# Performance work log

Measured on AMD Instinct MI355X. Metric: run time of the kernel, lower is better.

The kernel has to match this reference:

```python
import jax, jax.numpy as jnp
import numpy as np

D_MODEL = 1024
N_HEADS = 16
D_K = 64  # per-head dim and the scaling denominator used by the module
NEG = -1e9  # stand-in for -inf in masked_fill (rows are never fully masked)


def setup_inputs() -> dict:
    key = jax.random.key(0)
    ks = jax.random.split(key, 8)
    B, M, N = 2, 2048, 2048
    q = jax.random.normal(ks[0], (B, M, D_MODEL), dtype=jnp.float32)
    k = jax.random.normal(ks[1], (B, N, D_MODEL), dtype=jnp.float32)
    v = jax.random.normal(ks[2], (B, N, D_MODEL), dtype=jnp.float32)
    mask = jax.random.randint(ks[3], (B, M, N), 0, 2).astype(jnp.bool_)
    # xavier_uniform for square [d,d] weights: limit = sqrt(6/(d+d))
    lim = float(np.sqrt(6.0 / (D_MODEL + D_MODEL)))
    Wq = jax.random.uniform(ks[4], (D_MODEL, D_MODEL), jnp.float32, -lim, lim)
    Wk = jax.random.uniform(ks[5], (D_MODEL, D_MODEL), jnp.float32, -lim, lim)
    Wv = jax.random.uniform(ks[6], (D_MODEL, D_MODEL), jnp.float32, -lim, lim)
    Wo = jax.random.uniform(ks[7], (D_MODEL, D_MODEL), jnp.float32, -lim, lim)
    return {"q": q, "k": k, "v": v, "mask": mask,
            "Wq": Wq, "Wk": Wk, "Wv": Wv, "Wo": Wo}


def _split_heads(x):
    # (B, S, D) -> (B, H, S, Dh); the torch split/cat-on-batch trick is
    # mathematically identical to this standard head reshape.
    B, S, _ = x.shape
    return x.reshape(B, S, N_HEADS, D_K).transpose(0, 2, 1, 3)


def reference(q, k, v, mask, Wq, Wk, Wv, Wo):
    qw = _split_heads(q @ Wq.T)  # (B,H,M,Dh)
    kw = _split_heads(k @ Wk.T)  # (B,H,N,Dh)
    vw = _split_heads(v @ Wv.T)  # (B,H,N,Dh)
    scores = jnp.einsum('bhmd,bhnd->bhmn', qw, kw)
    scores = jnp.where(mask[:, None, :, :], NEG, scores)
    attn = jax.nn.softmax(scores / jnp.sqrt(jnp.float32(D_K)), axis=-1)
    ctx = jnp.einsum('bhmn,bhnd->bhmd', attn, vw)
    B, _, M, _ = ctx.shape
    ctx = ctx.transpose(0, 2, 1, 3).reshape(B, M, D_MODEL)
    return ctx @ Wo.T
```

## Files before the change

### kernel.cpp

```cpp
#include <hip/hip_runtime.h>
#include <hip/hip_bf16.h>
#include <stdint.h>
#include <string.h>

#define SEQ   2048
#define DM    1024
#define NH    16
#define NB    2

typedef __attribute__((ext_vector_type(8))) short bf16x8;
typedef __attribute__((ext_vector_type(4))) float f32x4;
typedef unsigned short u16;
typedef unsigned int   u32;

__device__ __forceinline__ u16 f2bf(float f) {
    u32 u = __float_as_uint(f);
    u += 0x7FFF + ((u >> 16) & 1);
    return (u16)(u >> 16);
}
__device__ __forceinline__ u32 pk2bf(float a, float b) {
    __hip_bfloat162 p = __float22bfloat162_rn(make_float2(a, b));
    u32 u; memcpy(&u, &p, 4); return u;
}
__device__ __forceinline__ float fexp2(float x) {
#if __has_builtin(__builtin_amdgcn_exp2f)
    return __builtin_amdgcn_exp2f(x);
#else
    return exp2f(x);
#endif
}
__device__ __forceinline__ void gl_lds16(const void* g, void* l) {
    __builtin_amdgcn_global_load_lds(
        (const __attribute__((address_space(1))) u32*)g,
        (__attribute__((address_space(3))) u32*)l, 16, 0, 0);
}
__device__ __forceinline__ void wbar_vm3() { asm volatile("s_waitcnt vmcnt(3)\ns_barrier" ::: "memory"); }
__device__ __forceinline__ void wbar_vm4() { asm volatile("s_waitcnt vmcnt(4)\ns_barrier" ::: "memory"); }
__device__ __forceinline__ void wbar_vm6() { asm volatile("s_waitcnt vmcnt(6)\ns_barrier" ::: "memory"); }
__device__ __forceinline__ void vm_drain() { asm volatile("s_waitcnt vmcnt(0)" ::: "memory"); }

struct CvtArgs {
    const float* s[7];
    u16* d[7];
    float scale[7];
    int start[8];
};
__global__ __launch_bounds__(256) void cvt_kernel(CvtArgs a) {
    int bid = blockIdx.x;
    int seg = 0;
#pragma unroll
    for (int i = 1; i < 7; ++i) if (bid >= a.start[i]) seg = i;
    float sc = a.scale[seg];
    size_t base = (size_t)(bid - a.start[seg]) * 2048 + threadIdx.x * 8;
    const float4* s4 = (const float4*)(a.s[seg] + base);
    float4 x = s4[0], y = s4[1];
    u32 r[4];
    r[0] = pk2bf(x.x*sc, x.y*sc); r[1] = pk2bf(x.z*sc, x.w*sc);
    r[2] = pk2bf(y.x*sc, y.y*sc); r[3] = pk2bf(y.z*sc, y.w*sc);
    *(uint4*)(a.d[seg] + base) = *(uint4*)r;
}

__global__ void maskpack_kernel(const int* __restrict__ mask,
                                unsigned int* __restrict__ bits) {
    int gid = blockIdx.x * 256 + threadIdx.x;
    int m = mask[gid];
    unsigned long long bal = __ballot(m != 0);
    int lane = threadIdx.x & 63;
    if (lane == 0)       bits[gid >> 5] = (u32)(bal & 0xFFFFFFFFull);
    else if (lane == 32) bits[gid >> 5] = (u32)(bal >> 32);
}

template<int RT>
__device__ __forceinline__ void gemm_body(const u16* __restrict__ A,
                                          const u16* __restrict__ Bm,
                                          void* __restrict__ Y,
                                          int rtile, int ctile, int mode,
                                          u16* sA, u16* sB) {
    constexpr int ABUF = RT * 32 * 32;
    constexpr int BBUF = 128 * 32;
    const int tid  = threadIdx.x;
    const int wv   = tid >> 6, lane = tid & 63;
    const int quad = lane >> 4, ln = lane & 15;
    const int wr   = wv >> 1,  wc  = wv & 1;

    const int lr4 = lane >> 2;
    const int lcc = ((lane & 3) ^ ((lane >> 3) & 3)) * 8;

    const u16* gA[RT/2]; u16* lA[RT/2];
#pragma unroll
    for (int s = 0; s < RT/2; ++s) {
        int seg = wv * (RT/2) + s;
        gA[s] = A + (size_t)(rtile * (RT*32) + seg*16 + lr4) * 1024 + lcc;
        lA[s] = sA + seg * 512;
    }
    const u16* gB[2]; u16* lB[2];
#pragma unroll
    for (int s = 0; s < 2; ++s) {
        int seg = wv * 2 + s;
        gB[s] = Bm + (size_t)(ctile * 128 + seg*16 + lr4) * 1024 + lcc;
        lB[s] = sB + seg * 512;
    }

    f32x4 acc[RT][4];
#pragma unroll
    for (int i = 0; i < RT; ++i)
#pragma unroll
        for (int j = 0; j < 4; ++j) acc[i][j] = (f32x4){0.f,0.f,0.f,0.f};

    const int c0 = (quad ^ ((ln >> 1) & 3)) * 8;

#pragma unroll
    for (int s = 0; s < RT/2; ++s) gl_lds16(gA[s], lA[s]);
#pragma unroll
    for (int s = 0; s < 2; ++s)    gl_lds16(gB[s], lB[s]);
#pragma unroll
    for (int s = 0; s < RT/2; ++s) gl_lds16(gA[s] + 32, lA[s] + ABUF);
#pragma unroll
    for (int s = 0; s < 2; ++s)    gl_lds16(gB[s] + 32, lB[s] + BBUF);

    int bc = 0, bp = 2;
    for (int kt = 0; kt < 32; ++kt) {
        if (RT == 4) wbar_vm4(); else wbar_vm3();
        int pk = (kt + 2) & 31;
#pragma unroll
        for (int s = 0; s < RT/2; ++s) gl_lds16(gA[s] + pk*32, lA[s] + bp*ABUF);
#pragma unroll
        for (int s = 0; s < 2; ++s)    gl_lds16(gB[s] + pk*32, lB[s] + bp*BBUF);

        const u16* sAb = sA + bc * ABUF;
        const u16* sBb = sB + bc * BBUF;
        bf16x8 af[RT], bfr[4];
#pragma unroll
        for (int rt = 0; rt < RT; ++rt)
            af[rt] = *(const bf16x8*)(sAb + (wr*(RT*16) + rt*16 + ln) * 32 + c0);
#pragma unroll
        for (int ct = 0; ct < 4; ++ct)
            bfr[ct] = *(const bf16x8*)(sBb + (wc*64 + ct*16 + ln) * 32 + c0);
#pragma unroll
        for (int rt = 0; rt < RT; ++rt)
#pragma unroll
            for (int ct = 0; ct < 4; ++ct)
                acc[rt][ct] = __builtin_amdgcn_mfma_f32_16x16x32_bf16(
                    af[rt], bfr[ct], acc[rt][ct], 0, 0, 0);

        bc = (bc == 2) ? 0 : bc + 1;
        bp = (bp == 2) ? 0 : bp + 1;
    }
    vm_drain();

#pragma unroll
    for (int rt = 0; rt < RT; ++rt) {
#pragma unroll
        for (int ct = 0; ct < 4; ++ct) {
#pragma unroll
            for (int i = 0; i < 4; ++i) {
                int R = rtile*(RT*32) + wr*(RT*16) + rt*16 + quad*4 + i;
                int C = ctile*128 + wc*64 + ct*16 + ln;
                float val = acc[rt][ct][i];
                if (mode == 0) {
                    int b = R >> 11, s = R & 2047, h = C >> 6, d = C & 63;
                    ((u16*)Y)[((size_t)((b*NH + h) * SEQ + s) << 6) + d] = f2bf(val);
                } else if (mode == 1) {
                    int h = R >> 6, d = R & 63, b = C >> 11, n = C & 2047;
                    ((u16*)Y)[((size_t)((b*NH + h) * 64 + d) << 11) + n] = f2bf(val);
                } else {
                    ((float*)Y)[(size_t)R * 1024 + C] = val;
                }
            }
        }
    }
}

struct QKVArgs { const u16* A[3]; const u16* B[3]; u16* Y[3]; };

__global__ __launch_bounds__(256) void gemm_qkv(QKVArgs g) {
    __shared__ u16 sA[3 * 128 * 32];
    __shared__ u16 sB[3 * 128 * 32];
    int z = blockIdx.z;
    if (z == 2)
        gemm_body<4>(g.A[2], g.B[2], g.Y[2], blockIdx.y, blockIdx.x, 1, sA, sB);
    else
        gemm_body<4>(g.A[z], g.B[z], g.Y[z], blockIdx.x, blockIdx.y, 0, sA, sB);
}

__global__ __launch_bounds__(256) void gemm_out(const u16* __restrict__ A,
                                                const u16* __restrict__ Bm,
                                                float* __restrict__ Y) {
    __shared__ u16 sA[3 * 64 * 32];
    __shared__ u16 sB[3 * 128 * 32];
    gemm_body<2>(A, Bm, Y, blockIdx.x, blockIdx.y, 2, sA, sB);
}

__global__ __launch_bounds__(256) void attn_kernel(
    const u16* __restrict__ qw,
    const u16* __restrict__ kw,
    const u16* __restrict__ vt,
    const u32* __restrict__ mbits,
    u16* __restrict__ ctx) {

    constexpr int RSD = 36;
    __shared__ u16 sK[3 * 4096];
    __shared__ u16 sV[3 * 4096];
    __shared__ u32 sPd[4 * 32 * RSD];

    const int mtile = blockIdx.x;
    const int bh    = blockIdx.y;
    const int b     = bh >> 4;
    const int tid   = threadIdx.x;
    const int wv    = tid >> 6, lane = tid & 63;
    const int quad  = lane >> 4, ln = lane & 15;
    const int m0    = mtile * 128;

    const size_t hbase = (size_t)bh * SEQ * 64;

    bf16x8 qf[2][2];
#pragma unroll
    for (int mt = 0; mt < 2; ++mt) {
        const u16* qp = qw + hbase + (size_t)(m0 + wv*32 + mt*16 + ln) * 64 + quad*8;
        qf[mt][0] = *(const bf16x8*)(qp);
        qf[mt][1] = *(const bf16x8*)(qp + 32);
    }

    f32x4 o[2][4], lsum[2];
#pragma unroll
    for (int mt = 0; mt < 2; ++mt) {
        lsum[mt] = (f32x4){0.f,0.f,0.f,0.f};
#pragma unroll
        for (int j = 0; j < 4; ++j) o[mt][j] = (f32x4){0.f,0.f,0.f,0.f};
    }

    bf16x8 ones;
#pragma unroll
    for (int i = 0; i < 8; ++i) ones[i] = (short)0x3F80;

    const u32* mrow[2];
#pragma unroll
    for (int mt = 0; mt < 2; ++mt)
        mrow[mt] = mbits + (size_t)(b*SEQ + m0 + wv*32 + mt*16 + ln) * 64;

    const int lr = lane >> 3;
    const int lc = (lane & 7) ^ lr;
    const u16* gK[2]; const u16* gV[2];
    u16 *lK[2], *lV[2];
#pragma unroll
    for (int s = 0; s < 2; ++s) {
        int seg = s * 4 + wv;
        gK[s] = kw + hbase + (size_t)(seg*8 + lr) * 64 + lc*8;
        gV[s] = vt + hbase + (size_t)(seg*8 + lr) * SEQ + lc*8;
        lK[s] = sK + seg * 512;
        lV[s] = sV + seg * 512;
    }

    const int c0 = (quad ^ (ln & 7)) * 8;
    u32* sPw = sPd + wv * 32 * RSD;
    const u16* sP16 = (const u16*)sPd;

#pragma unroll
    for (int s = 0; s < 2; ++s) { gl_lds16(gK[s], lK[s]); gl_lds16(gV[s], lV[s]); }
    uint2 wwA[2], wwB[2], wwC[2];
#pragma unroll
    for (int mt = 0; mt < 2; ++mt) wwA[mt] = *(const uint2*)(mrow[mt]);
#pragma unroll
    for (int s = 0; s < 2; ++s) {
        gl_lds16(gK[s] + 4096, lK[s] + 4096);
        gl_lds16(gV[s] + 64,   lV[s] + 4096);
    }
#pragma unroll
    for (int mt = 0; mt < 2; ++mt) wwB[mt] = *(const uint2*)(mrow[mt] + 2);

    int bc = 0, bp = 2;
    for (int nt = 0; nt < SEQ / 64; ++nt) {
        wbar_vm6();
        int pidx = (nt + 2) & 31;
#pragma unroll
        for (int s = 0; s < 2; ++s) {
            gl_lds16(gK[s] + (size_t)pidx * 4096, lK[s] + bp*4096);
            gl_lds16(gV[s] + pidx * 64,           lV[s] + bp*4096);
        }
#pragma unroll
        for (int mt = 0; mt < 2; ++mt)
            wwC[mt] = *(const uint2*)(mrow[mt] + pidx*2);

        const u16* sKb = sK + bc * 4096;
        const u16* sVb = sV + bc * 4096;

        f32x4 s4[2][4];
#pragma unroll
        for (int ct = 0; ct < 4; ++ct) {
            const u16* kp = sKb + (ct*16 + ln) * 64;
            bf16x8 k0 = *(const bf16x8*)(kp + c0);
            bf16x8 k1 = *(const bf16x8*)(kp + (c0 ^ 32));
#pragma unroll
            for (int mt = 0; mt < 2; ++mt) {
                f32x4 z = (f32x4){0.f, 0.f, 0.f, 0.f};
                z = __builtin_amdgcn_mfma_f32_16x16x32_bf16(k0, qf[mt][0], z, 0, 0, 0);
                z = __builtin_amdgcn_mfma_f32_16x16x32_bf16(k1, qf[mt][1], z, 0, 0, 0);
                s4[mt][ct] = z;
            }
        }

#pragma unroll
        for (int mt = 0; mt < 2; ++mt) {
            u32 w0 = wwA[mt].x >> (quad * 4);
            u32 w1 = wwA[mt].y >> (quad * 4);
#pragma unroll
            for (int ct = 0; ct < 4; ++ct) {
                u32 wsel = (ct & 2) ? w1 : w0;
                float p[4];
#pragma unroll
                for (int i = 0; i < 4; ++i) {
                    bool msk = (wsel >> ((ct & 1) * 16 + i)) & 1u;
                    p[i] = fexp2(msk ? -1e9f : s4[mt][ct][i]);
                }
                uint2 pk;
                pk.x = pk2bf(p[0], p[1]);
                pk.y = pk2bf(p[2], p[3]);
                *(uint2*)(sPw + (mt*16 + ln) * RSD + ct*8 + quad*2) = pk;
            }
        }

#pragma unroll
        for (int mt = 0; mt < 2; ++mt) {
            const u16* pp = sP16 + (wv*32 + mt*16 + ln) * 72;
            bf16x8 pf0 = *(const bf16x8*)(pp + quad*8);
            bf16x8 pf1 = *(const bf16x8*)(pp + 32 + quad*8);
            lsum[mt] = __builtin_amdgcn_mfma_f32_16x16x32_bf16(pf0, ones, lsum[mt], 0, 0, 0);
            lsum[mt] = __builtin_amdgcn_mfma_f32_16x16x32_bf16(pf1, ones, lsum[mt], 0, 0, 0);
#pragma unroll
            for (int ct = 0; ct < 4; ++ct) {
                const u16* vp = sVb + (ct*16 + ln) * 64;
                bf16x8 v0 = *(const bf16x8*)(vp + c0);
                bf16x8 v1 = *(const bf16x8*)(vp + (c0 ^ 32));
                o[mt][ct] = __builtin_amdgcn_mfma_f32_16x16x32_bf16(pf0, v0, o[mt][ct], 0, 0, 0);
                o[mt][ct] = __builtin_amdgcn_mfma_f32_16x16x32_bf16(pf1, v1, o[mt][ct], 0, 0, 0);
            }
        }

        wwA[0] = wwB[0]; wwA[1] = wwB[1];
        wwB[0] = wwC[0]; wwB[1] = wwC[1];
        bc = (bc == 2) ? 0 : bc + 1;
        bp = (bp == 2) ? 0 : bp + 1;
    }
    vm_drain();

#pragma unroll
    for (int mt = 0; mt < 2; ++mt)
#pragma unroll
        for (int i = 0; i < 4; ++i) {
            float inv = 1.f / lsum[mt][i];
            int m = m0 + wv*32 + mt*16 + quad*4 + i;
            size_t base = ((size_t)(b * SEQ + m) << 10) + (bh & 15) * 64;
#pragma unroll
            for (int ct = 0; ct < 4; ++ct)
                ctx[base + ct*16 + ln] = f2bf(o[mt][ct][i] * inv);
        }
}

extern "C" void kernel_launch(void* const* d_in, const int* in_sizes, int n_in,
                              void* d_out, int out_size, void* d_ws, size_t ws_size,
                              hipStream_t stream) {
    const float* q    = (const float*)d_in[0];
    const float* k    = (const float*)d_in[1];
    const float* v    = (const float*)d_in[2];
    const int*   mask = (const int*)d_in[3];
    const float* Wq   = (const float*)d_in[4];
    const float* Wk   = (const float*)d_in[5];
    const float* Wv   = (const float*)d_in[6];
    const float* Wo   = (const float*)d_in[7];
    float* out = (float*)d_out;

    char* ws = (char*)d_ws;
    const size_t SZH = (size_t)NB * SEQ * DM * 2;
    const size_t SZW = (size_t)DM * DM * 2;
    u16* qw   = (u16*)(ws);
    u16* kw   = (u16*)(ws + SZH);
    u16* vt   = (u16*)(ws + 2*SZH);
    u16* ctx  = (u16*)(ws + 3*SZH);
    u16* vb   = ctx;
    u32* mbits= (u32*)(ws + 4*SZH);
    u16* qb   = (u16*)(ws + 4*SZH + (1u<<20));
    u16* kb   = (u16*)(ws + 4*SZH + (1u<<20) + SZH);
    u16* Wqb  = (u16*)(ws + 4*SZH + (1u<<20) + 2*SZH);
    u16* Wkb  = (u16*)((char*)Wqb + SZW);
    u16* Wvb  = (u16*)((char*)Wqb + 2*SZW);
    u16* Wob  = (u16*)((char*)Wqb + 3*SZW);

    const float CSC = 0.18033688011112042f;

    CvtArgs ca;
    ca.s[0]=q;  ca.d[0]=qb;  ca.scale[0]=1.f;
    ca.s[1]=k;  ca.d[1]=kb;  ca.scale[1]=1.f;
    ca.s[2]=v;  ca.d[2]=vb;  ca.scale[2]=1.f;
    ca.s[3]=Wq; ca.d[3]=Wqb; ca.scale[3]=CSC;
    ca.s[4]=Wk; ca.d[4]=Wkb; ca.scale[4]=1.f;
    ca.s[5]=Wv; ca.d[5]=Wvb; ca.scale[5]=1.f;
    ca.s[6]=Wo; ca.d[6]=Wob; ca.scale[6]=1.f;
    int st[8] = {0, 2048, 4096, 6144, 6656, 7168, 7680, 8192};
    for (int i = 0; i < 8; ++i) ca.start[i] = st[i];
    cvt_kernel<<<dim3(8192), dim3(256), 0, stream>>>(ca);

    maskpack_kernel<<<dim3(NB*SEQ*SEQ/256), dim3(256), 0, stream>>>(mask, mbits);

    QKVArgs ga;
    ga.A[0]=qb;  ga.B[0]=Wqb; ga.Y[0]=qw;
    ga.A[1]=kb;  ga.B[1]=Wkb; ga.Y[1]=kw;
    ga.A[2]=Wvb; ga.B[2]=vb;  ga.Y[2]=vt;
    gemm_qkv<<<dim3(32, 8, 3), dim3(256), 0, stream>>>(ga);

    attn_kernel<<<dim3(SEQ/128, NB*NH), dim3(256), 0, stream>>>(qw, kw, vt, mbits, ctx);

    gemm_out<<<dim3(64, 8), dim3(256), 0, stream>>>(ctx, Wob, out);
}
```

Measured before the change: 276.3 us.

## Shrink attention M-tile to 64, double-buffer K/V, fuse convert and maskpack

The attention kernel now handles 64 query rows per block instead of 128, with one 16-row tile per wave. This doubles the grid to 1024 blocks and reduces registers and LDS per block, aimed at better occupancy and CU fill. The K/V prefetch drops from triple to double buffering, so less latency is hidden and each K/V tile is reused by fewer query rows, which doubles K/V traffic. The fp32-to-bf16 conversion and mask bit-packing kernels are merged into one launch to save a kernel launch and its tail.

```diff
diff --git a/kernel.cpp b/kernel.cpp
--- a/kernel.cpp
+++ b/kernel.cpp
@@ -34,9 +34,9 @@
         (const __attribute__((address_space(1))) u32*)g,
         (__attribute__((address_space(3))) u32*)l, 16, 0, 0);
 }
+__device__ __forceinline__ void wbar_vm1() { asm volatile("s_waitcnt vmcnt(1)\ns_barrier" ::: "memory"); }
 __device__ __forceinline__ void wbar_vm3() { asm volatile("s_waitcnt vmcnt(3)\ns_barrier" ::: "memory"); }
 __device__ __forceinline__ void wbar_vm4() { asm volatile("s_waitcnt vmcnt(4)\ns_barrier" ::: "memory"); }
-__device__ __forceinline__ void wbar_vm6() { asm volatile("s_waitcnt vmcnt(6)\ns_barrier" ::: "memory"); }
 __device__ __forceinline__ void vm_drain() { asm volatile("s_waitcnt vmcnt(0)" ::: "memory"); }
 
 struct CvtArgs {
@@ -45,29 +45,30 @@
     float scale[7];
     int start[8];
 };
-__global__ __launch_bounds__(256) void cvt_kernel(CvtArgs a) {
+__global__ __launch_bounds__(256) void prep_kernel(CvtArgs a,
+                                                   const int* __restrict__ mask,
+                                                   u32* __restrict__ bits) {
     int bid = blockIdx.x;
-    int seg = 0;
-#pragma unroll
-    for (int i = 1; i < 7; ++i) if (bid >= a.start[i]) seg = i;
-    float sc = a.scale[seg];
-    size_t base = (size_t)(bid - a.start[seg]) * 2048 + threadIdx.x * 8;
-    const float4* s4 = (const float4*)(a.s[seg] + base);
-    float4 x = s4[0], y = s4[1];
-    u32 r[4];
-    r[0] = pk2bf(x.x*sc, x.y*sc); r[1] = pk2bf(x.z*sc, x.w*sc);
-    r[2] = pk2bf(y.x*sc, y.y*sc); r[3] = pk2bf(y.z*sc, y.w*sc);
-    *(uint4*)(a.d[seg] + base) = *(uint4*)r;
-}
-
-__global__ void maskpack_kernel(const int* __restrict__ mask,
-                                unsigned int* __restrict__ bits) {
-    int gid = blockIdx.x * 256 + threadIdx.x;
-    int m = mask[gid];
-    unsigned long long bal = __ballot(m != 0);
-    int lane = threadIdx.x & 63;
-    if (lane == 0)       bits[gid >> 5] = (u32)(bal & 0xFFFFFFFFull);
-    else if (lane == 32) bits[gid >> 5] = (u32)(bal >> 32);
+    if (bid < 8192) {
+        int seg = 0;
+#pragma unroll
+        for (int i = 1; i < 7; ++i) if (bid >= a.start[i]) seg = i;
+        float sc = a.scale[seg];
+        size_t base = (size_t)(bid - a.start[seg]) * 2048 + threadIdx.x * 8;
+        const float4* s4 = (const float4*)(a.s[seg] + base);
+        float4 x = s4[0], y = s4[1];
+        u32 r[4];
+        r[0] = pk2bf(x.x*sc, x.y*sc); r[1] = pk2bf(x.z*sc, x.w*sc);
+        r[2] = pk2bf(y.x*sc, y.y*sc); r[3] = pk2bf(y.z*sc, y.w*sc);
+        *(uint4*)(a.d[seg] + base) = *(uint4*)r;
+    } else {
+        int gid = (bid - 8192) * 256 + threadIdx.x;
+        int m = mask[gid];
+        unsigned long long bal = __ballot(m != 0);
+        int lane = threadIdx.x & 63;
+        if (lane == 0)       bits[gid >> 5] = (u32)(bal & 0xFFFFFFFFull);
+        else if (lane == 32) bits[gid >> 5] = (u32)(bal >> 32);
+    }
 }
 
 template<int RT>
@@ -198,10 +199,10 @@
     const u32* __restrict__ mbits,
     u16* __restrict__ ctx) {
 
-    constexpr int RSD = 36;
-    __shared__ u16 sK[3 * 4096];
-    __shared__ u16 sV[3 * 4096];
-    __shared__ u32 sPd[4 * 32 * RSD];
+    constexpr int RSD = 34;
+    __shared__ u16 sK[2 * 4096];
+    __shared__ u16 sV[2 * 4096];
+    __shared__ u32 sPd[4 * 16 * RSD];
 
     const int mtile = blockIdx.x;
     const int bh    = blockIdx.y;
@@ -209,34 +210,27 @@
     const int tid   = threadIdx.x;
     const int wv    = tid >> 6, lane = tid & 63;
     const int quad  = lane >> 4, ln = lane & 15;
-    const int m0    = mtile * 128;
+    const int m0    = mtile * 64;
 
     const size_t hbase = (size_t)bh * SEQ * 64;
 
-    bf16x8 qf[2][2];
-#pragma unroll
-    for (int mt = 0; mt < 2; ++mt) {
-        const u16* qp = qw + hbase + (size_t)(m0 + wv*32 + mt*16 + ln) * 64 + quad*8;
-        qf[mt][0] = *(const bf16x8*)(qp);
-        qf[mt][1] = *(const bf16x8*)(qp + 32);
-    }
-
-    f32x4 o[2][4], lsum[2];
-#pragma unroll
-    for (int mt = 0; mt < 2; ++mt) {
-        lsum[mt] = (f32x4){0.f,0.f,0.f,0.f};
-#pragma unroll
-        for (int j = 0; j < 4; ++j) o[mt][j] = (f32x4){0.f,0.f,0.f,0.f};
-    }
+    bf16x8 qf0, qf1;
+    {
+        const u16* qp = qw + hbase + (size_t)(m0 + wv*16 + ln) * 64 + quad*8;
+        qf0 = *(const bf16x8*)(qp);
+        qf1 = *(const bf16x8*)(qp + 32);
+    }
+
+    f32x4 o[4], lsum;
+#pragma unroll
+    for (int j = 0; j < 4; ++j) o[j] = (f32x4){0.f,0.f,0.f,0.f};
+    lsum = (f32x4){0.f,0.f,0.f,0.f};
 
     bf16x8 ones;
 #pragma unroll
     for (int i = 0; i < 8; ++i) ones[i] = (short)0x3F80;
 
-    const u32* mrow[2];
-#pragma unroll
-    for (int mt = 0; mt < 2; ++mt)
-        mrow[mt] = mbits + (size_t)(b*SEQ + m0 + wv*32 + mt*16 + ln) * 64;
+    const u32* mrow = mbits + (size_t)(b*SEQ + m0 + wv*16 + ln) * 64;
 
     const int lr = lane >> 3;
     const int lc = (lane & 7) ^ lr;
@@ -252,57 +246,42 @@
     }
 
     const int c0 = (quad ^ (ln & 7)) * 8;
-    u32* sPw = sPd + wv * 32 * RSD;
-    const u16* sP16 = (const u16*)sPd;
+    u32* sPw = sPd + wv * 16 * RSD;
+    const u16* sP16 = (const u16*)sPw;
 
 #pragma unroll
     for (int s = 0; s < 2; ++s) { gl_lds16(gK[s], lK[s]); gl_lds16(gV[s], lV[s]); }
-    uint2 wwA[2], wwB[2], wwC[2];
-#pragma unroll
-    for (int mt = 0; mt < 2; ++mt) wwA[mt] = *(const uint2*)(mrow[mt]);
-#pragma unroll
-    for (int s = 0; s < 2; ++s) {
-        gl_lds16(gK[s] + 4096, lK[s] + 4096);
-        gl_lds16(gV[s] + 64,   lV[s] + 4096);
-    }
-#pragma unroll
-    for (int mt = 0; mt < 2; ++mt) wwB[mt] = *(const uint2*)(mrow[mt] + 2);
-
-    int bc = 0, bp = 2;
+    uint2 wwA = *(const uint2*)(mrow);
+
     for (int nt = 0; nt < SEQ / 64; ++nt) {
-        wbar_vm6();
-        int pidx = (nt + 2) & 31;
+        wbar_vm1();
+        const int pidx = (nt + 1) & 31;
+        const int bc = nt & 1, bp = pidx & 1;
 #pragma unroll
         for (int s = 0; s < 2; ++s) {
             gl_lds16(gK[s] + (size_t)pidx * 4096, lK[s] + bp*4096);
             gl_lds16(gV[s] + pidx * 64,           lV[s] + bp*4096);
         }
-#pragma unroll
-        for (int mt = 0; mt < 2; ++mt)
-            wwC[mt] = *(const uint2*)(mrow[mt] + pidx*2);
+        uint2 wwB = *(const uint2*)(mrow + pidx*2);
 
         const u16* sKb = sK + bc * 4096;
         const u16* sVb = sV + bc * 4096;
 
-        f32x4 s4[2][4];
+        f32x4 s4[4];
 #pragma unroll
         for (int ct = 0; ct < 4; ++ct) {
             const u16* kp = sKb + (ct*16 + ln) * 64;
             bf16x8 k0 = *(const bf16x8*)(kp + c0);
             bf16x8 k1 = *(const bf16x8*)(kp + (c0 ^ 32));
-#pragma unroll
-            for (int mt = 0; mt < 2; ++mt) {
-                f32x4 z = (f32x4){0.f, 0.f, 0.f, 0.f};
-                z = __builtin_amdgcn_mfma_f32_16x16x32_bf16(k0, qf[mt][0], z, 0, 0, 0);
-                z = __builtin_amdgcn_mfma_f32_16x16x32_bf16(k1, qf[mt][1], z, 0, 0, 0);
-                s4[mt][ct] = z;
-            }
-        }
-
-#pragma unroll
-        for (int mt = 0; mt < 2; ++mt) {
-            u32 w0 = wwA[mt].x >> (quad * 4);
-            u32 w1 = wwA[mt].y >> (quad * 4);
+            f32x4 z = (f32x4){0.f, 0.f, 0.f, 0.f};
+            z = __builtin_amdgcn_mfma_f32_16x16x32_bf16(k0, qf0, z, 0, 0, 0);
+            z = __builtin_amdgcn_mfma_f32_16x16x32_bf16(k1, qf1, z, 0, 0, 0);
+            s4[ct] = z;
+        }
+
+        {
+            u32 w0 = wwA.x >> (quad * 4);
+            u32 w1 = wwA.y >> (quad * 4);
 #pragma unroll
             for (int ct = 0; ct < 4; ++ct) {
                 u32 wsel = (ct & 2) ? w1 : w0;
@@ -310,50 +289,42 @@
 #pragma unroll
                 for (int i = 0; i < 4; ++i) {
                     bool msk = (wsel >> ((ct & 1) * 16 + i)) & 1u;
-                    p[i] = fexp2(msk ? -1e9f : s4[mt][ct][i]);
+                    p[i] = fexp2(msk ? -1e9f : s4[ct][i]);
                 }
                 uint2 pk;
                 pk.x = pk2bf(p[0], p[1]);
                 pk.y = pk2bf(p[2], p[3]);
-                *(uint2*)(sPw + (mt*16 + ln) * RSD + ct*8 + quad*2) = pk;
+                *(uint2*)(sPw + ln * RSD + ct*8 + quad*2) = pk;
             }
         }
 
-#pragma unroll
-        for (int mt = 0; mt < 2; ++mt) {
-            const u16* pp = sP16 + (wv*32 + mt*16 + ln) * 72;
-            bf16x8 pf0 = *(const bf16x8*)(pp + quad*8);
-            bf16x8 pf1 = *(const bf16x8*)(pp + 32 + quad*8);
-            lsum[mt] = __builtin_amdgcn_mfma_f32_16x16x32_bf16(pf0, ones, lsum[mt], 0, 0, 0);
-            lsum[mt] = __builtin_amdgcn_mfma_f32_16x16x32_bf16(pf1, ones, lsum[mt], 0, 0, 0);
-#pragma unroll
-            for (int ct = 0; ct < 4; ++ct) {
-                const u16* vp = sVb + (ct*16 + ln) * 64;
-                bf16x8 v0 = *(const bf16x8*)(vp + c0);
-                bf16x8 v1 = *(const bf16x8*)(vp + (c0 ^ 32));
-                o[mt][ct] = __builtin_amdgcn_mfma_f32_16x16x32_bf16(pf0, v0, o[mt][ct], 0, 0, 0);
-                o[mt][ct] = __builtin_amdgcn_mfma_f32_16x16x32_bf16(pf1, v1, o[mt][ct], 0, 0, 0);
-            }
-        }
-
-        wwA[0] = wwB[0]; wwA[1] = wwB[1];
-        wwB[0] = wwC[0]; wwB[1] = wwC[1];
-        bc = (bc == 2) ? 0 : bc + 1;
-        bp = (bp == 2) ? 0 : bp + 1;
+        const u16* pp = sP16 + ln * 68;
+        bf16x8 pf0 = *(const bf16x8*)(pp + quad*8);
+        bf16x8 pf1 = *(const bf16x8*)(pp + 32 + quad*8);
+        lsum = __builtin_amdgcn_mfma_f32_16x16x32_bf16(pf0, ones, lsum, 0, 0, 0);
+        lsum = __builtin_amdgcn_mfma_f32_16x16x32_bf16(pf1, ones, lsum, 0, 0, 0);
+#pragma unroll
+        for (int ct = 0; ct < 4; ++ct) {
+            const u16* vp = sVb + (ct*16 + ln) * 64;
+            bf16x8 v0 = *(const bf16x8*)(vp + c0);
+            bf16x8 v1 = *(const bf16x8*)(vp + (c0 ^ 32));
+            o[ct] = __builtin_amdgcn_mfma_f32_16x16x32_bf16(pf0, v0, o[ct], 0, 0, 0);
+            o[ct] = __builtin_amdgcn_mfma_f32_16x16x32_bf16(pf1, v1, o[ct], 0, 0, 0);
+        }
+
+        wwA = wwB;
     }
     vm_drain();
 
 #pragma unroll
-    for (int mt = 0; mt < 2; ++mt)
-#pragma unroll
-        for (int i = 0; i < 4; ++i) {
-            float inv = 1.f / lsum[mt][i];
-            int m = m0 + wv*32 + mt*16 + quad*4 + i;
-            size_t base = ((size_t)(b * SEQ + m) << 10) + (bh & 15) * 64;
-#pragma unroll
-            for (int ct = 0; ct < 4; ++ct)
-                ctx[base + ct*16 + ln] = f2bf(o[mt][ct][i] * inv);
-        }
+    for (int i = 0; i < 4; ++i) {
+        float inv = 1.f / lsum[i];
+        int m = m0 + wv*16 + quad*4 + i;
+        size_t base = ((size_t)(b * SEQ + m) << 10) + (bh & 15) * 64;
+#pragma unroll
+        for (int ct = 0; ct < 4; ++ct)
+            ctx[base + ct*16 + ln] = f2bf(o[ct][i] * inv);
+    }
 }
 
 extern "C" void kernel_launch(void* const* d_in, const int* in_sizes, int n_in,
@@ -397,9 +368,8 @@
     ca.s[6]=Wo; ca.d[6]=Wob; ca.scale[6]=1.f;
     int st[8] = {0, 2048, 4096, 6144, 6656, 7168, 7680, 8192};
     for (int i = 0; i < 8; ++i) ca.start[i] = st[i];
-    cvt_kernel<<<dim3(8192), dim3(256), 0, stream>>>(ca);
-
-    maskpack_kernel<<<dim3(NB*SEQ*SEQ/256), dim3(256), 0, stream>>>(mask, mbits);
+
+    prep_kernel<<<dim3(8192 + NB*SEQ*SEQ/256), dim3(256), 0, stream>>>(ca, mask, mbits);
 
     QKVArgs ga;
     ga.A[0]=qb;  ga.B[0]=Wqb; ga.Y[0]=qw;
@@ -407,7 +377,7 @@
     ga.A[2]=Wvb; ga.B[2]=vb;  ga.Y[2]=vt;
     gemm_qkv<<<dim3(32, 8, 3), dim3(256), 0, stream>>>(ga);
 
-    attn_kernel<<<dim3(SEQ/128, NB*NH), dim3(256), 0, stream>>>(qw, kw, vt, mbits, ctx);
+    attn_kernel<<<dim3(SEQ/64, NB*NH), dim3(256), 0, stream>>>(qw, kw, vt, mbits, ctx);
 
     gemm_out<<<dim3(64, 8), dim3(256), 0, stream>>>(ctx, Wob, out);
 }
```

Measured after the change: 313.3 us. 1.13x slower.
